# Optimization experiments

Hardware: AMD Instinct MI355X
Metric: run time of the kernel (lower is better)

The kernel has to match this reference:

```python
import jax, jax.numpy as jnp
import numpy as np

GAMMA = 0.5
K = 3
SKIP_THRESHOLD = 1.0


def setup_inputs() -> dict:
    key = jax.random.key(0)
    ks = jax.random.split(key, 11)
    in_dim, out_dim, mem_len = 1024, 128, 131072
    inp = {
        "x": jax.random.normal(ks[0], (1, in_dim), jnp.float32),
        "mean": jax.random.normal(ks[1], (in_dim,), jnp.float32),
        "std": jax.random.uniform(ks[2], (in_dim,), jnp.float32, 0.5, 1.5),
        "memory": jax.random.normal(ks[3], (mem_len, out_dim), jnp.float32),
        "mem_data": jax.random.normal(ks[4], (mem_len, in_dim), jnp.float32),
        "W_enc": jax.random.normal(ks[5], (in_dim, out_dim), jnp.float32) * 0.02,
        "b_enc": jnp.zeros((out_dim,), jnp.float32),
        "W_dec": jax.random.normal(ks[6], (out_dim, in_dim), jnp.float32) * 0.02,
        "b_dec": jnp.zeros((in_dim,), jnp.float32),
        "win_mean": jnp.zeros((), jnp.float32),   # WindowLoss running mean
        "win_std": jnp.ones((), jnp.float32),     # WindowLoss sample std (1 if population_std==0)
    }
    return inp


def reference(x, mean, std, memory, mem_data, W_enc, b_enc, W_dec, b_dec, win_mean, win_std):
    # normalize: new = (x - mean) / std, zero where std == 0
    new = jnp.where(std == 0, 0.0, (x - mean) / std)            # [1, in_dim]
    # encoder: Linear + Tanh
    enc = jnp.tanh(new @ W_enc + b_enc)                          # [1, out_dim]
    # window_loss: decoder reconstruction MSE, gated by ndtr of z-scored loss
    rec = enc @ W_dec + b_dec                                    # [1, in_dim]
    mse = jnp.mean((rec - new) ** 2)                             # scalar
    prob = jax.scipy.special.ndtr((mse - win_mean) / win_std)    # torch uses loss.item() -> constant
    win_loss = (SKIP_THRESHOLD - prob) / SKIP_THRESHOLD * mse
    # L1-distance top-k (smallest) against the memory bank
    dist = jnp.sum(jnp.abs(memory - enc), axis=1)                # [mem_len]
    neg_d, idx = jax.lax.top_k(-dist, K)
    distances = -neg_d                                           # [K] smallest distances
    expw = GAMMA ** jnp.arange(K, dtype=jnp.float32)
    loss_values = jnp.sum(distances * expw) / jnp.sum(expw)
    # conditional FIFO scatter update at the nearest index
    cond = loss_values <= win_loss
    i0 = idx[0]
    new_memory = jnp.where(cond, memory.at[i0].set(enc[0]), memory)
    new_mem_data = jnp.where(cond, mem_data.at[i0].set(x[0]), mem_data)
    loss_combined = win_loss + loss_values
    return loss_combined, new_memory, new_mem_data
```

## Files before the change

kernel.cpp:

```cpp
#include <hip/hip_runtime.h>
#include <math.h>
#include <float.h>

#define IN_DIM   1024
#define OUT_DIM  128
#define MEM_LEN  131072
#define COPY_GRID 2048
#define DIST_BLOCKS 2048

#define NA_FLOATS  ((long long)MEM_LEN * OUT_DIM)
#define NB_FLOATS  ((long long)MEM_LEN * IN_DIM)
#define N_TOTAL    (NA_FLOATS + NB_FLOATS)
#define NFRAMES    (N_TOTAL / 1024)
#define FRAME_MEM  16384

__device__ __forceinline__ void ins3(float v, int i,
    float& v0, int& i0, float& v1, int& i1, float& v2, int& i2) {
  if (v < v0 || (v == v0 && i < i0)) {
    v2 = v1; i2 = i1; v1 = v0; i1 = i0; v0 = v; i0 = i;
  } else if (v < v1 || (v == v1 && i < i1)) {
    v2 = v1; i2 = i1; v1 = v; i1 = i;
  } else if (v < v2 || (v == v2 && i < i2)) {
    v2 = v; i2 = i;
  }
}

__global__ __launch_bounds__(1024) void k1_encode(
    const float* __restrict__ x, const float* __restrict__ mean,
    const float* __restrict__ stdv, const float* __restrict__ W_enc,
    const float* __restrict__ b_enc, const float* __restrict__ W_dec,
    const float* __restrict__ b_dec, const float* __restrict__ win_mean,
    const float* __restrict__ win_std,
    float* __restrict__ ws_enc, float* __restrict__ ws_winloss) {
  __shared__ float s_new[IN_DIM];
  __shared__ float s_part[8][OUT_DIM];
  __shared__ float s_enc[OUT_DIM];
  __shared__ float s_red[16];
  const int t = threadIdx.x;
  const float sd = stdv[t];
  const float nv = (sd == 0.0f) ? 0.0f : (x[t] - mean[t]) / sd;
  s_new[t] = nv;
  __syncthreads();
  const int o = t & (OUT_DIM - 1);
  const int p = t >> 7;
  float partial = 0.0f;
  #pragma unroll 8
  for (int i = 0; i < 128; ++i) {
    const int k = p * 128 + i;
    partial += s_new[k] * W_enc[k * OUT_DIM + o];
  }
  s_part[p][o] = partial;
  __syncthreads();
  if (t < OUT_DIM) {
    float sum = b_enc[t];
    #pragma unroll
    for (int pp = 0; pp < 8; ++pp) sum += s_part[pp][t];
    const float e = tanhf(sum);
    s_enc[t] = e;
    ws_enc[t] = e;
  }
  __syncthreads();
  float r = b_dec[t];
  #pragma unroll 8
  for (int k = 0; k < OUT_DIM; ++k) r += s_enc[k] * W_dec[k * IN_DIM + t];
  const float diff = r - nv;
  float sq = diff * diff;
  for (int off = 32; off; off >>= 1) sq += __shfl_xor(sq, off, 64);
  const int lane = t & 63, wid = t >> 6;
  if (lane == 0) s_red[wid] = sq;
  __syncthreads();
  if (t == 0) {
    float tot = 0.0f;
    #pragma unroll
    for (int w = 0; w < 16; ++w) tot += s_red[w];
    const float mse = tot / (float)IN_DIM;
    const float z = (mse - win_mean[0]) / win_std[0];
    const float prob = 0.5f * erfcf(-z * 0.70710678118654752440f);
    ws_winloss[0] = (1.0f - prob) * mse;
  }
}

__global__ __launch_bounds__(256) void k2_dist(
    const float* __restrict__ memory, const float* __restrict__ ws_enc,
    float* __restrict__ topv, int* __restrict__ topi) {
  const int t = threadIdx.x;
  const int lane = t & 63;
  const int wid = t >> 6;
  const int half = lane >> 5;
  const int col  = lane & 31;
  const float4 e = reinterpret_cast<const float4*>(ws_enc)[col];
  const float4* m4 = reinterpret_cast<const float4*>(memory);
  float v0 = FLT_MAX, v1 = FLT_MAX, v2 = FLT_MAX;
  int i0 = 0x7fffffff, i1 = 0x7fffffff, i2 = 0x7fffffff;
  const int r0 = (blockIdx.x * 4 + wid) * 16;
  for (int rr = 0; rr < 16; rr += 2) {
    const float4 m = m4[(size_t)(r0 + rr) * 32 + lane];
    float d = fabsf(m.x - e.x) + fabsf(m.y - e.y)
            + fabsf(m.z - e.z) + fabsf(m.w - e.w);
    d += __shfl_xor(d, 1, 64);
    d += __shfl_xor(d, 2, 64);
    d += __shfl_xor(d, 4, 64);
    d += __shfl_xor(d, 8, 64);
    d += __shfl_xor(d, 16, 64);
    ins3(d, r0 + rr + half, v0, i0, v1, i1, v2, i2);
  }
  {
    const float w0 = __shfl_xor(v0, 32, 64);
    const float w1 = __shfl_xor(v1, 32, 64);
    const float w2 = __shfl_xor(v2, 32, 64);
    const int j0 = __shfl_xor(i0, 32, 64);
    const int j1 = __shfl_xor(i1, 32, 64);
    const int j2 = __shfl_xor(i2, 32, 64);
    ins3(w0, j0, v0, i0, v1, i1, v2, i2);
    ins3(w1, j1, v0, i0, v1, i1, v2, i2);
    ins3(w2, j2, v0, i0, v1, i1, v2, i2);
  }
  __shared__ float sv[4][3];
  __shared__ int   si[4][3];
  if (lane == 0) {
    sv[wid][0] = v0; sv[wid][1] = v1; sv[wid][2] = v2;
    si[wid][0] = i0; si[wid][1] = i1; si[wid][2] = i2;
  }
  __syncthreads();
  if (t == 0) {
    for (int w = 1; w < 4; ++w)
      for (int j = 0; j < 3; ++j)
        ins3(sv[w][j], si[w][j], v0, i0, v1, i1, v2, i2);
    topv[blockIdx.x * 3 + 0] = v0; topi[blockIdx.x * 3 + 0] = i0;
    topv[blockIdx.x * 3 + 1] = v1; topi[blockIdx.x * 3 + 1] = i1;
    topv[blockIdx.x * 3 + 2] = v2; topi[blockIdx.x * 3 + 2] = i2;
  }
}

__global__ __launch_bounds__(256) void copy_all(
    const float* __restrict__ memory, const float* __restrict__ mem_data,
    float* __restrict__ out) {
  const int t = threadIdx.x;
  const int lane = t & 63;
  const int wid  = t >> 6;
  const float4* mem4 = reinterpret_cast<const float4*>(memory);
  const float4* md4  = reinterpret_cast<const float4*>(mem_data);
  float4* out4 = reinterpret_cast<float4*>(out);
  const long long wstride = (long long)gridDim.x * 4;
  for (long long s = (long long)blockIdx.x * 4 + wid; s < NFRAMES; s += wstride) {
    const float4* src4 = (s < FRAME_MEM) ? (mem4 + (s << 8))
                                         : (md4 + ((s - FRAME_MEM) << 8));
    float edge = 0.0f;
    if (s > 0) {
      const long long sd = (s << 10) - 1;
      edge = (sd < NA_FLOATS) ? memory[sd] : mem_data[sd - NA_FLOATS];
    }
    const float4 a0 = src4[lane];
    const float4 a1 = src4[lane + 64];
    const float4 a2 = src4[lane + 128];
    const float4 a3 = src4[lane + 192];
    float p0 = __shfl_up(a0.w, 1, 64);
    float p1 = __shfl_up(a1.w, 1, 64);
    float p2 = __shfl_up(a2.w, 1, 64);
    float p3 = __shfl_up(a3.w, 1, 64);
    const float t1 = __shfl(a0.w, 63, 64);
    const float t2 = __shfl(a1.w, 63, 64);
    const float t3 = __shfl(a2.w, 63, 64);
    if (lane == 0) { p0 = edge; p1 = t1; p2 = t2; p3 = t3; }
    float4* ob = out4 + (s << 8);
    ob[lane]       = make_float4(p0, a0.x, a0.y, a0.z);
    ob[lane + 64]  = make_float4(p1, a1.x, a1.y, a1.z);
    ob[lane + 128] = make_float4(p2, a2.x, a2.y, a2.z);
    ob[lane + 192] = make_float4(p3, a3.x, a3.y, a3.z);
  }
  if (blockIdx.x == 0 && t == 0)
    out[N_TOTAL] = mem_data[NB_FLOATS - 1];
}

__global__ __launch_bounds__(1024) void k3_topk_update(
    const float* __restrict__ topv, const int* __restrict__ topi,
    const float* __restrict__ ws_winloss, const float* __restrict__ ws_enc,
    const float* __restrict__ x, float* __restrict__ out_loss,
    float* __restrict__ out_mem, float* __restrict__ out_md) {
  const int t = threadIdx.x;
  const int n = DIST_BLOCKS * 3;
  float v0 = FLT_MAX, v1 = FLT_MAX, v2 = FLT_MAX;
  int i0 = 0x7fffffff, i1 = 0x7fffffff, i2 = 0x7fffffff;
  for (int j = t; j < n; j += 1024) ins3(topv[j], topi[j], v0, i0, v1, i1, v2, i2);
  for (int off = 32; off; off >>= 1) {
    const float ov0 = __shfl_xor(v0, off, 64);
    const float ov1 = __shfl_xor(v1, off, 64);
    const float ov2 = __shfl_xor(v2, off, 64);
    const int oi0 = __shfl_xor(i0, off, 64);
    const int oi1 = __shfl_xor(i1, off, 64);
    const int oi2 = __shfl_xor(i2, off, 64);
    ins3(ov0, oi0, v0, i0, v1, i1, v2, i2);
    ins3(ov1, oi1, v0, i0, v1, i1, v2, i2);
    ins3(ov2, oi2, v0, i0, v1, i1, v2, i2);
  }
  __shared__ float sv[16][3];
  __shared__ int   si[16][3];
  __shared__ int s_i0, s_cond;
  const int lane = t & 63, wid = t >> 6;
  if (lane == 0) {
    sv[wid][0] = v0; sv[wid][1] = v1; sv[wid][2] = v2;
    si[wid][0] = i0; si[wid][1] = i1; si[wid][2] = i2;
  }
  __syncthreads();
  if (t == 0) {
    for (int w = 1; w < 16; ++w)
      for (int j = 0; j < 3; ++j)
        ins3(sv[w][j], si[w][j], v0, i0, v1, i1, v2, i2);
    const float loss_values = (v0 + 0.5f * v1 + 0.25f * v2) / 1.75f;
    const float wl = ws_winloss[0];
    out_loss[0] = wl + loss_values;
    s_i0 = i0;
    s_cond = (loss_values <= wl) ? 1 : 0;
  }
  __syncthreads();
  if (s_cond) {
    if (t < OUT_DIM) out_mem[(size_t)s_i0 * OUT_DIM + t] = ws_enc[t];
    out_md[(size_t)s_i0 * IN_DIM + t] = x[t];
  }
}

extern "C" void kernel_launch(void* const* d_in, const int* in_sizes, int n_in,
                              void* d_out, int out_size, void* d_ws, size_t ws_size,
                              hipStream_t stream) {
  const float* x        = (const float*)d_in[0];
  const float* mean     = (const float*)d_in[1];
  const float* stdv     = (const float*)d_in[2];
  const float* memory   = (const float*)d_in[3];
  const float* mem_data = (const float*)d_in[4];
  const float* W_enc    = (const float*)d_in[5];
  const float* b_enc    = (const float*)d_in[6];
  const float* W_dec    = (const float*)d_in[7];
  const float* b_dec    = (const float*)d_in[8];
  const float* win_mean = (const float*)d_in[9];
  const float* win_std  = (const float*)d_in[10];

  float* out      = (float*)d_out;
  float* out_loss = out;
  float* out_mem  = out + 1;
  float* out_md   = out + 1 + (size_t)MEM_LEN * OUT_DIM;

  float* ws        = (float*)d_ws;
  float* ws_enc    = ws;
  float* ws_wl     = ws + 128;
  float* ws_topv   = ws + 256;
  int*   ws_topi   = (int*)(ws + 256 + DIST_BLOCKS * 3);

  k1_encode<<<1, 1024, 0, stream>>>(x, mean, stdv, W_enc, b_enc, W_dec, b_dec,
                                    win_mean, win_std, ws_enc, ws_wl);
  k2_dist<<<DIST_BLOCKS, 256, 0, stream>>>(memory, ws_enc, ws_topv, ws_topi);
  copy_all<<<COPY_GRID, 256, 0, stream>>>(memory, mem_data, out);
  k3_topk_update<<<1, 1024, 0, stream>>>(ws_topv, ws_topi, ws_wl, ws_enc, x,
                                         out_loss, out_mem, out_md);
}
```

Before: 327.8 us.

## Split encoder across blocks, move decoder off critical path, nontemporal paired copy

The single-block encode/decode kernel is split in two. The encoder now runs as 128 blocks, one per output, with wave reductions. The decoder MSE runs as 8 blocks after the distance kernel and writes partial sums, and the final kernel finishes the window-loss computation. The copy kernel now moves two frames per wave iteration with nontemporal stores on half the grid, to raise memory-level parallelism and avoid cache pollution. This adds one more launch, and the encoder kernel reads W_enc with a strided pattern.

```diff
diff --git a/kernel.cpp b/kernel.cpp
--- a/kernel.cpp
+++ b/kernel.cpp
@@ -5,14 +5,17 @@
 #define IN_DIM   1024
 #define OUT_DIM  128
 #define MEM_LEN  131072
-#define COPY_GRID 2048
+#define COPY_GRID 1024
 #define DIST_BLOCKS 2048
 
 #define NA_FLOATS  ((long long)MEM_LEN * OUT_DIM)
 #define NB_FLOATS  ((long long)MEM_LEN * IN_DIM)
 #define N_TOTAL    (NA_FLOATS + NB_FLOATS)
 #define NFRAMES    (N_TOTAL / 1024)
+#define NPAIRS     (NFRAMES / 2)
 #define FRAME_MEM  16384
+
+typedef float f4 __attribute__((ext_vector_type(4)));
 
 __device__ __forceinline__ void ins3(float v, int i,
     float& v0, int& i0, float& v1, int& i1, float& v2, int& i2) {
@@ -25,59 +28,49 @@
   }
 }
 
-__global__ __launch_bounds__(1024) void k1_encode(
+__global__ __launch_bounds__(256) void k1a_enc(
     const float* __restrict__ x, const float* __restrict__ mean,
     const float* __restrict__ stdv, const float* __restrict__ W_enc,
-    const float* __restrict__ b_enc, const float* __restrict__ W_dec,
-    const float* __restrict__ b_dec, const float* __restrict__ win_mean,
-    const float* __restrict__ win_std,
-    float* __restrict__ ws_enc, float* __restrict__ ws_winloss) {
-  __shared__ float s_new[IN_DIM];
-  __shared__ float s_part[8][OUT_DIM];
+    const float* __restrict__ b_enc, float* __restrict__ ws_enc) {
+  const int o = blockIdx.x;
+  const int t = threadIdx.x;
+  float partial = 0.0f;
+  #pragma unroll
+  for (int j = 0; j < 4; ++j) {
+    const int k = t + 256 * j;
+    const float sd = stdv[k];
+    const float nv = (sd == 0.0f) ? 0.0f : (x[k] - mean[k]) / sd;
+    partial += nv * W_enc[k * OUT_DIM + o];
+  }
+  for (int off = 32; off; off >>= 1) partial += __shfl_xor(partial, off, 64);
+  __shared__ float s[4];
+  if ((t & 63) == 0) s[t >> 6] = partial;
+  __syncthreads();
+  if (t == 0) ws_enc[o] = tanhf(s[0] + s[1] + s[2] + s[3] + b_enc[o]);
+}
+
+__global__ __launch_bounds__(128) void k1b_dec(
+    const float* __restrict__ x, const float* __restrict__ mean,
+    const float* __restrict__ stdv, const float* __restrict__ W_dec,
+    const float* __restrict__ b_dec, const float* __restrict__ ws_enc,
+    float* __restrict__ ws_sse) {
+  const int t = threadIdx.x;
+  const int o = blockIdx.x * 128 + t;
   __shared__ float s_enc[OUT_DIM];
-  __shared__ float s_red[16];
-  const int t = threadIdx.x;
-  const float sd = stdv[t];
-  const float nv = (sd == 0.0f) ? 0.0f : (x[t] - mean[t]) / sd;
-  s_new[t] = nv;
-  __syncthreads();
-  const int o = t & (OUT_DIM - 1);
-  const int p = t >> 7;
-  float partial = 0.0f;
+  s_enc[t] = ws_enc[t];
+  __syncthreads();
+  float r = b_dec[o];
   #pragma unroll 8
-  for (int i = 0; i < 128; ++i) {
-    const int k = p * 128 + i;
-    partial += s_new[k] * W_enc[k * OUT_DIM + o];
-  }
-  s_part[p][o] = partial;
-  __syncthreads();
-  if (t < OUT_DIM) {
-    float sum = b_enc[t];
-    #pragma unroll
-    for (int pp = 0; pp < 8; ++pp) sum += s_part[pp][t];
-    const float e = tanhf(sum);
-    s_enc[t] = e;
-    ws_enc[t] = e;
-  }
-  __syncthreads();
-  float r = b_dec[t];
-  #pragma unroll 8
-  for (int k = 0; k < OUT_DIM; ++k) r += s_enc[k] * W_dec[k * IN_DIM + t];
+  for (int k = 0; k < OUT_DIM; ++k) r += s_enc[k] * W_dec[k * IN_DIM + o];
+  const float sd = stdv[o];
+  const float nv = (sd == 0.0f) ? 0.0f : (x[o] - mean[o]) / sd;
   const float diff = r - nv;
   float sq = diff * diff;
   for (int off = 32; off; off >>= 1) sq += __shfl_xor(sq, off, 64);
-  const int lane = t & 63, wid = t >> 6;
-  if (lane == 0) s_red[wid] = sq;
-  __syncthreads();
-  if (t == 0) {
-    float tot = 0.0f;
-    #pragma unroll
-    for (int w = 0; w < 16; ++w) tot += s_red[w];
-    const float mse = tot / (float)IN_DIM;
-    const float z = (mse - win_mean[0]) / win_std[0];
-    const float prob = 0.5f * erfcf(-z * 0.70710678118654752440f);
-    ws_winloss[0] = (1.0f - prob) * mse;
-  }
+  __shared__ float sr[2];
+  if ((t & 63) == 0) sr[t >> 6] = sq;
+  __syncthreads();
+  if (t == 0) ws_sse[blockIdx.x] = sr[0] + sr[1];
 }
 
 __global__ __launch_bounds__(256) void k2_dist(
@@ -138,35 +131,66 @@
   const int t = threadIdx.x;
   const int lane = t & 63;
   const int wid  = t >> 6;
-  const float4* mem4 = reinterpret_cast<const float4*>(memory);
-  const float4* md4  = reinterpret_cast<const float4*>(mem_data);
-  float4* out4 = reinterpret_cast<float4*>(out);
+  const f4* mem4 = reinterpret_cast<const f4*>(memory);
+  const f4* md4  = reinterpret_cast<const f4*>(mem_data);
+  f4* out4 = reinterpret_cast<f4*>(out);
   const long long wstride = (long long)gridDim.x * 4;
-  for (long long s = (long long)blockIdx.x * 4 + wid; s < NFRAMES; s += wstride) {
-    const float4* src4 = (s < FRAME_MEM) ? (mem4 + (s << 8))
-                                         : (md4 + ((s - FRAME_MEM) << 8));
+  for (long long P = (long long)blockIdx.x * 4 + wid; P < NPAIRS; P += wstride) {
+    const long long sA = 2 * P;
+    const f4* srcA = (sA < FRAME_MEM) ? (mem4 + (sA << 8))
+                                      : (md4 + ((sA - FRAME_MEM) << 8));
+    const f4* srcB = srcA + 256;
     float edge = 0.0f;
-    if (s > 0) {
-      const long long sd = (s << 10) - 1;
+    if (P > 0) {
+      const long long sd = (sA << 10) - 1;
       edge = (sd < NA_FLOATS) ? memory[sd] : mem_data[sd - NA_FLOATS];
     }
-    const float4 a0 = src4[lane];
-    const float4 a1 = src4[lane + 64];
-    const float4 a2 = src4[lane + 128];
-    const float4 a3 = src4[lane + 192];
+    const f4 a0 = srcA[lane];
+    const f4 a1 = srcA[lane + 64];
+    const f4 a2 = srcA[lane + 128];
+    const f4 a3 = srcA[lane + 192];
+    const f4 b0 = srcB[lane];
+    const f4 b1 = srcB[lane + 64];
+    const f4 b2 = srcB[lane + 128];
+    const f4 b3 = srcB[lane + 192];
     float p0 = __shfl_up(a0.w, 1, 64);
     float p1 = __shfl_up(a1.w, 1, 64);
     float p2 = __shfl_up(a2.w, 1, 64);
     float p3 = __shfl_up(a3.w, 1, 64);
-    const float t1 = __shfl(a0.w, 63, 64);
-    const float t2 = __shfl(a1.w, 63, 64);
-    const float t3 = __shfl(a2.w, 63, 64);
-    if (lane == 0) { p0 = edge; p1 = t1; p2 = t2; p3 = t3; }
-    float4* ob = out4 + (s << 8);
-    ob[lane]       = make_float4(p0, a0.x, a0.y, a0.z);
-    ob[lane + 64]  = make_float4(p1, a1.x, a1.y, a1.z);
-    ob[lane + 128] = make_float4(p2, a2.x, a2.y, a2.z);
-    ob[lane + 192] = make_float4(p3, a3.x, a3.y, a3.z);
+    float q0 = __shfl_up(b0.w, 1, 64);
+    float q1 = __shfl_up(b1.w, 1, 64);
+    float q2 = __shfl_up(b2.w, 1, 64);
+    float q3 = __shfl_up(b3.w, 1, 64);
+    const float tA1 = __shfl(a0.w, 63, 64);
+    const float tA2 = __shfl(a1.w, 63, 64);
+    const float tA3 = __shfl(a2.w, 63, 64);
+    const float tB0 = __shfl(a3.w, 63, 64);
+    const float tB1 = __shfl(b0.w, 63, 64);
+    const float tB2 = __shfl(b1.w, 63, 64);
+    const float tB3 = __shfl(b2.w, 63, 64);
+    if (lane == 0) {
+      p0 = edge; p1 = tA1; p2 = tA2; p3 = tA3;
+      q0 = tB0;  q1 = tB1; q2 = tB2; q3 = tB3;
+    }
+    f4* oA = out4 + (sA << 8);
+    f4 w;
+    w.x = p0; w.y = a0.x; w.z = a0.y; w.w = a0.z;
+    __builtin_nontemporal_store(w, oA + lane);
+    w.x = p1; w.y = a1.x; w.z = a1.y; w.w = a1.z;
+    __builtin_nontemporal_store(w, oA + lane + 64);
+    w.x = p2; w.y = a2.x; w.z = a2.y; w.w = a2.z;
+    __builtin_nontemporal_store(w, oA + lane + 128);
+    w.x = p3; w.y = a3.x; w.z = a3.y; w.w = a3.z;
+    __builtin_nontemporal_store(w, oA + lane + 192);
+    f4* oB = oA + 256;
+    w.x = q0; w.y = b0.x; w.z = b0.y; w.w = b0.z;
+    __builtin_nontemporal_store(w, oB + lane);
+    w.x = q1; w.y = b1.x; w.z = b1.y; w.w = b1.z;
+    __builtin_nontemporal_store(w, oB + lane + 64);
+    w.x = q2; w.y = b2.x; w.z = b2.y; w.w = b2.z;
+    __builtin_nontemporal_store(w, oB + lane + 128);
+    w.x = q3; w.y = b3.x; w.z = b3.y; w.w = b3.z;
+    __builtin_nontemporal_store(w, oB + lane + 192);
   }
   if (blockIdx.x == 0 && t == 0)
     out[N_TOTAL] = mem_data[NB_FLOATS - 1];
@@ -174,7 +198,8 @@
 
 __global__ __launch_bounds__(1024) void k3_topk_update(
     const float* __restrict__ topv, const int* __restrict__ topi,
-    const float* __restrict__ ws_winloss, const float* __restrict__ ws_enc,
+    const float* __restrict__ ws_sse, const float* __restrict__ win_mean,
+    const float* __restrict__ win_std, const float* __restrict__ ws_enc,
     const float* __restrict__ x, float* __restrict__ out_loss,
     float* __restrict__ out_mem, float* __restrict__ out_md) {
   const int t = threadIdx.x;
@@ -206,8 +231,14 @@
     for (int w = 1; w < 16; ++w)
       for (int j = 0; j < 3; ++j)
         ins3(sv[w][j], si[w][j], v0, i0, v1, i1, v2, i2);
+    float sse = 0.0f;
+    #pragma unroll
+    for (int b = 0; b < 8; ++b) sse += ws_sse[b];
+    const float mse = sse / (float)IN_DIM;
+    const float z = (mse - win_mean[0]) / win_std[0];
+    const float prob = 0.5f * erfcf(-z * 0.70710678118654752440f);
+    const float wl = (1.0f - prob) * mse;
     const float loss_values = (v0 + 0.5f * v1 + 0.25f * v2) / 1.75f;
-    const float wl = ws_winloss[0];
     out_loss[0] = wl + loss_values;
     s_i0 = i0;
     s_cond = (loss_values <= wl) ? 1 : 0;
@@ -241,14 +272,15 @@
 
   float* ws        = (float*)d_ws;
   float* ws_enc    = ws;
-  float* ws_wl     = ws + 128;
+  float* ws_sse    = ws + 128;
   float* ws_topv   = ws + 256;
   int*   ws_topi   = (int*)(ws + 256 + DIST_BLOCKS * 3);
 
-  k1_encode<<<1, 1024, 0, stream>>>(x, mean, stdv, W_enc, b_enc, W_dec, b_dec,
-                                    win_mean, win_std, ws_enc, ws_wl);
+  k1a_enc<<<OUT_DIM, 256, 0, stream>>>(x, mean, stdv, W_enc, b_enc, ws_enc);
   k2_dist<<<DIST_BLOCKS, 256, 0, stream>>>(memory, ws_enc, ws_topv, ws_topi);
+  k1b_dec<<<8, 128, 0, stream>>>(x, mean, stdv, W_dec, b_dec, ws_enc, ws_sse);
   copy_all<<<COPY_GRID, 256, 0, stream>>>(memory, mem_data, out);
-  k3_topk_update<<<1, 1024, 0, stream>>>(ws_topv, ws_topi, ws_wl, ws_enc, x,
+  k3_topk_update<<<1, 1024, 0, stream>>>(ws_topv, ws_topi, ws_sse, win_mean,
+                                         win_std, ws_enc, x,
                                          out_loss, out_mem, out_md);
 }
```

New measurement: 321.9 us. About the same (-1.8%).
